# Performance work log

Hardware: AMD Instinct MI355X
Metric: run time of the kernel (lower is better)

Reference implementation:

```python
import jax, jax.numpy as jnp
import numpy as np

HIDDEN = 4096
N_HEADS = 32
N_KV = 8
HEAD_DIM = 128
ROPE_THETA = 10000.0
B, S = 2, 2048


def _rope_neox(x, cos, sin):
    # x: [B,S,H,D]; cos/sin: [B,S,1,D/2]
    half = x.shape[-1] // 2
    x1, x2 = x[..., :half], x[..., half:]
    return jnp.concatenate([x1 * cos - x2 * sin, x2 * cos + x1 * sin], axis=-1)


def setup_inputs() -> dict:
    key = jax.random.key(0)
    k1, k2, k3 = jax.random.split(key, 3)
    hidden_states = jax.random.normal(k1, (B, S, HIDDEN), dtype=jnp.float32)
    positions = jnp.arange(B * S, dtype=jnp.int32).reshape(B, S)
    q_size = N_HEADS * HEAD_DIM
    kv_size = N_KV * HEAD_DIM
    w_qkv = jax.random.normal(k2, (HIDDEN, q_size + 2 * kv_size), dtype=jnp.float32) * (HIDDEN ** -0.5)
    w_o = jax.random.normal(k3, (q_size, HIDDEN), dtype=jnp.float32) * (q_size ** -0.5)
    return {"hidden_states": hidden_states, "positions": positions, "w_qkv": w_qkv, "w_o": w_o}


def reference(hidden_states, positions, w_qkv, w_o):
    q_size = N_HEADS * HEAD_DIM
    kv_size = N_KV * HEAD_DIM
    b, s, _ = hidden_states.shape

    qkv = hidden_states @ w_qkv  # [B,S,q+2kv]
    q = qkv[..., :q_size].reshape(b, s, N_HEADS, HEAD_DIM)
    k = qkv[..., q_size:q_size + kv_size].reshape(b, s, N_KV, HEAD_DIM)
    v = qkv[..., q_size + kv_size:].reshape(b, s, N_KV, HEAD_DIM)

    # RoPE (neox style, full rotary dim)
    inv_freq = 1.0 / (ROPE_THETA ** (jnp.arange(0, HEAD_DIM, 2, dtype=jnp.float32) / HEAD_DIM))
    ang = positions.astype(jnp.float32)[..., None] * inv_freq  # [B,S,D/2]
    cos = jnp.cos(ang)[:, :, None, :]
    sin = jnp.sin(ang)[:, :, None, :]
    q = _rope_neox(q, cos, sin)
    k = _rope_neox(k, cos, sin)

    # GQA: expand kv heads to match q heads
    rep = N_HEADS // N_KV
    k = jnp.repeat(k, rep, axis=2)  # [B,S,H,D]
    v = jnp.repeat(v, rep, axis=2)

    scale = HEAD_DIM ** -0.5
    scores = jnp.einsum('bqhd,bkhd->bhqk', q, k) * scale  # [B,H,S,S]
    causal = jnp.tril(jnp.ones((s, s), dtype=bool))
    scores = jnp.where(causal[None, None], scores, jnp.finfo(scores.dtype).min)
    probs = jax.nn.softmax(scores, axis=-1)
    attn = jnp.einsum('bhqk,bkhd->bqhd', probs, v).reshape(b, s, q_size)
    return attn @ w_o
```

## Files before the change

### kernel.cpp

```cpp
#include <hip/hip_runtime.h>
#include <hip/hip_bf16.h>
#include <stdint.h>
#include <stddef.h>

typedef unsigned short u16;
typedef __bf16 bf16x8 __attribute__((ext_vector_type(8)));
typedef float f32x4 __attribute__((ext_vector_type(4)));
typedef float f32x16 __attribute__((ext_vector_type(16)));
typedef unsigned u32x2 __attribute__((ext_vector_type(2)));

#define NH 32
#define NKV 8
#define HD 128
#define QKV_N 6144
#define SEQ 2048

__device__ __forceinline__ u16 f2b(float x) {
  union { float f; unsigned u; } v; v.f = x;
  unsigned r = v.u + 0x7FFF + ((v.u >> 16) & 1);
  return (u16)(r >> 16);
}
__device__ __forceinline__ float b2f(u16 b) {
  union { float f; unsigned u; } v; v.u = ((unsigned)b) << 16;
  return v.f;
}
__device__ __forceinline__ void gload16(const void* g, void* l) {
  __builtin_amdgcn_global_load_lds((const __attribute__((address_space(1))) unsigned int*)g,
                                   (__attribute__((address_space(3))) unsigned int*)l, 16, 0, 0);
}
template <int N>
__device__ __forceinline__ void vmwait() {
  asm volatile("s_waitcnt vmcnt(%0)" ::"n"(N) : "memory");
}
__device__ __forceinline__ unsigned pk(float lo, float hi) {
  union { __bf16 h[2]; unsigned w; } u;
  u.h[0] = (__bf16)lo; u.h[1] = (__bf16)hi;
  return u.w;
}
__device__ __forceinline__ void plswap(unsigned& a, unsigned& b) {
  u32x2 r = __builtin_amdgcn_permlane32_swap(a, b, false, false);
  a = r.x; b = r.y;
}
__device__ __forceinline__ float pl_partner_max(float x) {
  unsigned u = __float_as_uint(x);
  u32x2 r = __builtin_amdgcn_permlane32_swap(u, u, false, false);
  return fmaxf(__uint_as_float(r.x), __uint_as_float(r.y));
}
__device__ __forceinline__ float pl_partner_sum(float x) {
  unsigned u = __float_as_uint(x);
  u32x2 r = __builtin_amdgcn_permlane32_swap(u, u, false, false);
  return __uint_as_float(r.x) + __uint_as_float(r.y);
}

__global__ void cast_f32_bf16(const float* __restrict__ in, u16* __restrict__ out, int n) {
  int i = (blockIdx.x * blockDim.x + threadIdx.x) * 4;
  if (i >= n) return;
  float4 v = *(const float4*)&in[i];
  ushort4 o;
  o.x = f2b(v.x); o.y = f2b(v.y); o.z = f2b(v.z); o.w = f2b(v.w);
  *(ushort4*)&out[i] = o;
}

__global__ void cast_transpose(const float* __restrict__ in, u16* __restrict__ out, int K, int N) {
  __shared__ float t[32][33];
  int n0 = blockIdx.x * 32, k0 = blockIdx.y * 32;
  int tx = threadIdx.x, ty = threadIdx.y;
#pragma unroll
  for (int i = 0; i < 4; ++i)
    t[ty + i * 8][tx] = in[(size_t)(k0 + ty + i * 8) * N + n0 + tx];
  __syncthreads();
#pragma unroll
  for (int i = 0; i < 4; ++i)
    out[(size_t)(n0 + ty + i * 8) * K + k0 + tx] = f2b(t[tx][ty + i * 8]);
}

__device__ __forceinline__ void storeC(float* C, size_t i, float v) { C[i] = v; }
__device__ __forceinline__ void storeC(u16* C, size_t i, float v) { C[i] = f2b(v); }

#define MFMA16(q, A0, A1, B0, B1)                                                              \
  {                                                                                            \
    _Pragma("unroll") for (int mi = 0; mi < 4; ++mi)                                           \
      _Pragma("unroll") for (int ni = 0; ni < 2; ++ni)                                         \
        acc[q][mi][ni] = __builtin_amdgcn_mfma_f32_16x16x32_bf16(A0[mi], B0[ni], acc[q][mi][ni], 0, 0, 0); \
    _Pragma("unroll") for (int mi = 0; mi < 4; ++mi)                                           \
      _Pragma("unroll") for (int ni = 0; ni < 2; ++ni)                                         \
        acc[q][mi][ni] = __builtin_amdgcn_mfma_f32_16x16x32_bf16(A1[mi], B1[ni], acc[q][mi][ni], 0, 0, 0); \
  }

#define KTILE(NOFF, SGHI, SGLO, VMA, HASVMB, VMB)                                              \
  {                                                                                            \
    bf16x8 a0[4], a1[4], bl0[2], bl1[2], bh0[2], bh1[2];                                       \
                                  \
    _Pragma("unroll") for (int mi = 0; mi < 4; ++mi) {                                         \
      a0[mi] = *(const bf16x8*)(rA0 + (NOFF) + mi * 1024);                                     \
      a1[mi] = *(const bf16x8*)(rA1 + (NOFF) + mi * 1024);                                     \
    }                                                                                          \
    _Pragma("unroll") for (int ni = 0; ni < 2; ++ni) {                                         \
      bl0[ni] = *(const bf16x8*)(rB0 + (NOFF) + ni * 1024);                                    \
      bl1[ni] = *(const bf16x8*)(rB1 + (NOFF) + ni * 1024);                                    \
      bh0[ni] = *(const bf16x8*)(rB0 + (NOFF) + 8192 + ni * 1024);                             \
      bh1[ni] = *(const bf16x8*)(rB1 + (NOFF) + 8192 + ni * 1024);                             \
    }                                                                                          \
    if (SGHI) {                                                                                \
      gload16(pBhi0, dBhi0 + ((NOFF) ^ 16384)); gload16(pBhi1, dBhi1 + ((NOFF) ^ 16384));      \
      pBhi0 += 64; pBhi1 += 64;                                                                \
      gload16(pAhi0, dAhi0 + ((NOFF) ^ 16384)); gload16(pAhi1, dAhi1 + ((NOFF) ^ 16384));      \
      pAhi0 += 64; pAhi1 += 64;                                                                \
    }                                                                                          \
    __builtin_amdgcn_s_barrier();                                                              \
    __builtin_amdgcn_s_setprio(1);                                                             \
    MFMA16(0, a0, a1, bl0, bl1)                                                                \
    MFMA16(1, a0, a1, bh0, bh1)                                                                \
    __builtin_amdgcn_s_setprio(0);                                                             \
    __builtin_amdgcn_sched_barrier(0);                                                         \
    vmwait<VMA>();                                                                             \
    __builtin_amdgcn_s_barrier();                                                              \
                                         \
    _Pragma("unroll") for (int mi = 0; mi < 4; ++mi) {                                         \
      a0[mi] = *(const bf16x8*)(rA0 + (NOFF) + 8192 + mi * 1024);                              \
      a1[mi] = *(const bf16x8*)(rA1 + (NOFF) + 8192 + mi * 1024);                              \
    }                                                                                          \
    if (SGLO) {                                                                                \
      gload16(pAlo0, dAlo0 + (NOFF)); gload16(pAlo1, dAlo1 + (NOFF));                          \
      pAlo0 += 64; pAlo1 += 64;                                                                \
      gload16(pBlo0, dBlo0 + (NOFF)); gload16(pBlo1, dBlo1 + (NOFF));                          \
      pBlo0 += 64; pBlo1 += 64;                                                                \
    }                                                                                          \
    __builtin_amdgcn_s_barrier();                                                              \
    __builtin_amdgcn_s_setprio(1);                                                             \
    MFMA16(2, a0, a1, bl0, bl1)                                                                \
    MFMA16(3, a0, a1, bh0, bh1)                                                                \
    __builtin_amdgcn_s_setprio(0);                                                             \
    __builtin_amdgcn_sched_barrier(0);                                                         \
    if (HASVMB) vmwait<VMB>();                                                                 \
    __builtin_amdgcn_s_barrier();                                                              \
  }

template <typename OutT>
__global__ __launch_bounds__(512, 2) void gemm256(const u16* __restrict__ A, const u16* __restrict__ Bt,
                                                  OutT* __restrict__ C, int M, int N, int K) {
  __shared__ __align__(16) u16 sA[2 * 16384];
  __shared__ __align__(16) u16 sB[2 * 16384];
  const int nbx = N >> 8;
  const int nwg = (M >> 8) * nbx;
  const int cpx = nwg >> 3;
  const int wg = ((int)blockIdx.x & 7) * cpx + ((int)blockIdx.x >> 3);
  const int row0 = (wg / nbx) << 8, col0 = (wg % nbx) << 8;
  const int tid = threadIdx.x, w = tid >> 6, lane = tid & 63;
  const int wm = w >> 2, wn = w & 3;
  const int lq = lane & 15, lh = lane >> 4, x7 = lq & 7;
  const int o0 = (lh ^ x7) << 3, o1 = ((4 + lh) ^ x7) << 3;
  const int nt = K >> 6;

  const int rr = tid >> 3;
  const int swz = ((tid & 7) ^ (rr & 7)) << 3;
  const u16* pAlo0 = A + (size_t)(row0 + rr) * K + swz;
  const u16* pAlo1 = A + (size_t)(row0 + 64 + rr) * K + swz;
  const u16* pAhi0 = A + (size_t)(row0 + 128 + rr) * K + swz;
  const u16* pAhi1 = A + (size_t)(row0 + 192 + rr) * K + swz;
  const u16* pBlo0 = Bt + (size_t)(col0 + rr) * K + swz;
  const u16* pBlo1 = Bt + (size_t)(col0 + 64 + rr) * K + swz;
  const u16* pBhi0 = Bt + (size_t)(col0 + 128 + rr) * K + swz;
  const u16* pBhi1 = Bt + (size_t)(col0 + 192 + rr) * K + swz;
  u16* dAlo0 = sA + w * 512;
  u16* dAlo1 = sA + 4096 + w * 512;
  u16* dAhi0 = sA + 8192 + w * 512;
  u16* dAhi1 = sA + 12288 + w * 512;
  u16* dBlo0 = sB + w * 512;
  u16* dBlo1 = sB + 4096 + w * 512;
  u16* dBhi0 = sB + 8192 + w * 512;
  u16* dBhi1 = sB + 12288 + w * 512;
  const u16* rA0 = sA + (wm * 64 + lq) * 64 + o0;
  const u16* rA1 = sA + (wm * 64 + lq) * 64 + o1;
  const u16* rB0 = sB + (wn * 32 + lq) * 64 + o0;
  const u16* rB1 = sB + (wn * 32 + lq) * 64 + o1;

  f32x4 acc[4][4][2] = {};

  gload16(pAlo0, dAlo0); gload16(pAlo1, dAlo1); pAlo0 += 64; pAlo1 += 64;
  gload16(pBlo0, dBlo0); gload16(pBlo1, dBlo1); pBlo0 += 64; pBlo1 += 64;
  gload16(pBhi0, dBhi0); gload16(pBhi1, dBhi1); pBhi0 += 64; pBhi1 += 64;
  gload16(pAhi0, dAhi0); gload16(pAhi1, dAhi1); pAhi0 += 64; pAhi1 += 64;
  gload16(pAlo0, dAlo0 + 16384); gload16(pAlo1, dAlo1 + 16384); pAlo0 += 64; pAlo1 += 64;
  gload16(pBlo0, dBlo0 + 16384); gload16(pBlo1, dBlo1 + 16384); pBlo0 += 64; pBlo1 += 64;
  vmwait<6>();
  __builtin_amdgcn_s_barrier();

  for (int t = 0; t < nt - 2; t += 2) {
    KTILE(0, 1, 1, 8, 1, 6)
    KTILE(16384, 1, 1, 8, 1, 6)
  }
  KTILE(0, 1, 0, 8, 1, 2)
  KTILE(16384, 0, 0, 0, 0, 0)

#pragma unroll
  for (int q = 0; q < 4; ++q) {
    const int ah = q >> 1, bh2 = q & 1;
#pragma unroll
    for (int mi = 0; mi < 4; ++mi)
#pragma unroll
      for (int ni = 0; ni < 2; ++ni)
#pragma unroll
        for (int j = 0; j < 4; ++j) {
          const int row = row0 + ah * 128 + wm * 64 + mi * 16 + lh * 4 + j;
          const int col = col0 + bh2 * 128 + wn * 32 + ni * 16 + lq;
          storeC(C, (size_t)row * N + col, acc[q][mi][ni][j]);
        }
  }
}

__global__ void rope_kernel(u16* __restrict__ qkv, const int* __restrict__ pos, float qscale) {
  __shared__ float cs[64], sn[64];
  const int row = blockIdx.x;
  const int tid = threadIdx.x;
  if (tid < 64) {
    float p = (float)pos[row];
    float inv = exp2f(-(float)tid * 0.20762050593046f);
    float a = p * inv;
    cs[tid] = cosf(a);
    sn[tid] = sinf(a);
  }
  __syncthreads();
  const size_t base = (size_t)row * QKV_N;
  for (int i = tid; i < 40 * 64; i += 256) {
    const int h = i >> 6, d = i & 63;
    const size_t o = base + h * 128 + d;
    float x1 = b2f(qkv[o]), x2 = b2f(qkv[o + 64]);
    float c = cs[d], s = sn[d];
    float o1 = x1 * c - x2 * s;
    float o2 = x2 * c + x1 * s;
    if (h < NH) { o1 *= qscale; o2 *= qscale; }
    qkv[o] = f2b(o1);
    qkv[o + 64] = f2b(o2);
  }
}

__global__ void v_transpose(const u16* __restrict__ qkv, u16* __restrict__ vt) {
  __shared__ u16 t[32][33];
  const int b = blockIdx.z >> 3, kvh = blockIdx.z & 7;
  const int s0 = blockIdx.x * 32, d0 = blockIdx.y * 32;
  const int tx = threadIdx.x, ty = threadIdx.y;
#pragma unroll
  for (int i = 0; i < 4; ++i)
    t[ty + i * 8][tx] = qkv[(size_t)(b * SEQ + s0 + ty + i * 8) * QKV_N + 5120 + kvh * 128 + d0 + tx];
  __syncthreads();
#pragma unroll
  for (int i = 0; i < 4; ++i)
    vt[(size_t)((b * NKV + kvh) * HD + d0 + ty + i * 8) * SEQ + s0 + tx] = t[tx][ty + i * 8];
}

__global__ __launch_bounds__(512, 2) void attn_kernel(const u16* __restrict__ qkv, const u16* __restrict__ vt,
                                                      u16* __restrict__ attn) {
  __shared__ __align__(16) u16 sK[2][64 * 128];
  __shared__ __align__(16) u16 sV[2][128 * 64];
  const int b = blockIdx.z, h = blockIdx.y;
  const int qt = (b == 0) ? blockIdx.x : 7 - blockIdx.x;
  const int kvh = h >> 2;
  const int qb = qt * 256;
  const int tid = threadIdx.x, w = tid >> 6, lane = tid & 63;
  const int lq = lane & 31, hi = lane >> 5, x7 = lane & 7;
  const int qw = qb + (w << 5);
  const int qa = qw + lq;
  const int nt = 4 * (qt + 1);

  auto stage = [&](int buf, int kt) {
    const int k0 = kt * 64;
#pragma unroll
    for (int c = 0; c < 2; ++c) {
      const int g = c * 512 + tid;
      const int r = g >> 4, gc = g & 15;
      const int gs = gc ^ (r & 7);
      gload16(qkv + (size_t)(b * SEQ + k0 + r) * QKV_N + 4096 + kvh * 128 + gs * 8,
              &sK[buf][(c * 512 + (w << 6)) * 8]);
    }
#pragma unroll
    for (int c = 0; c < 2; ++c) {
      const int g = c * 512 + tid;
      const int r = g >> 3, gc = g & 7;
      const int gs = gc ^ (r & 7);
      gload16(vt + (size_t)((b * NKV + kvh) * HD + r) * SEQ + k0 + gs * 8,
              &sV[buf][(c * 512 + (w << 6)) * 8]);
    }
  };

  stage(0, 0);
  bf16x8 qf[8];
#pragma unroll
  for (int ks = 0; ks < 8; ++ks)
    qf[ks] = *(const bf16x8*)&qkv[(size_t)(b * SEQ + qw + lq) * QKV_N + h * 128 + ks * 16 + 8 * hi];

  f32x16 o[4] = {};
  float mreg = -1e30f, lreg = 0.f;

  asm volatile("s_waitcnt vmcnt(0)" ::: "memory");
  __builtin_amdgcn_s_barrier();

  for (int kt = 0; kt < nt; ++kt) {
    const int cur = kt & 1;
    const int k0 = kt * 64;
    if (kt + 1 < nt) {
      stage(cur ^ 1, kt + 1);
      asm volatile("s_waitcnt vmcnt(4)" ::: "memory");
    } else {
      asm volatile("s_waitcnt vmcnt(0)" ::: "memory");
    }
    __builtin_amdgcn_s_barrier();

    if (k0 <= qw + 31) {
      const u16* sk = sK[cur];
      f32x16 st0 = {}, st1 = {};
      __builtin_amdgcn_s_setprio(1);
#pragma unroll
      for (int ks = 0; ks < 8; ++ks) {
        const int g = ((2 * ks + hi) ^ x7) * 8;
        bf16x8 kf0 = *(const bf16x8*)&sk[lq * 128 + g];
        bf16x8 kf1 = *(const bf16x8*)&sk[(32 + lq) * 128 + g];
        st0 = __builtin_amdgcn_mfma_f32_32x32x16_bf16(kf0, qf[ks], st0, 0, 0, 0);
        st1 = __builtin_amdgcn_mfma_f32_32x32x16_bf16(kf1, qf[ks], st1, 0, 0, 0);
      }
      __builtin_amdgcn_s_setprio(0);
      if (k0 + 63 > qw) {
#pragma unroll
        for (int r = 0; r < 16; ++r) {
          const int cr = (r & 3) + 8 * (r >> 2) + 4 * hi;
          st0[r] = (k0 + cr <= qa) ? st0[r] : -1e30f;
          st1[r] = (k0 + 32 + cr <= qa) ? st1[r] : -1e30f;
        }
      }
      float a8[8];
#pragma unroll
      for (int r = 0; r < 8; ++r)
        a8[r] = fmaxf(fmaxf(st0[r], st0[r + 8]), fmaxf(st1[r], st1[r + 8]));
#pragma unroll
      for (int s = 4; s; s >>= 1)
#pragma unroll
        for (int r = 0; r < s; ++r) a8[r] = fmaxf(a8[r], a8[r + s]);
      const float pm = pl_partner_max(a8[0]);
      if (!__all(pm <= mreg + 8.f)) {
        const float mn = fmaxf(mreg, pm);
        const float al = exp2f(mreg - mn);
        lreg *= al;
        mreg = mn;
#pragma unroll
        for (int r = 0; r < 16; ++r) {
          const int cr = (r & 3) + 8 * (r >> 2) + 4 * hi;
          const float ar = __shfl(al, cr, 64);
#pragma unroll
          for (int dn = 0; dn < 4; ++dn) o[dn][r] *= ar;
        }
      }
#pragma unroll
      for (int r = 0; r < 16; ++r) {
        st0[r] = exp2f(st0[r] - mreg);
        st1[r] = exp2f(st1[r] - mreg);
      }
      float s8[8];
#pragma unroll
      for (int r = 0; r < 8; ++r)
        s8[r] = (st0[r] + st0[r + 8]) + (st1[r] + st1[r + 8]);
#pragma unroll
      for (int s = 4; s; s >>= 1)
#pragma unroll
        for (int r = 0; r < s; ++r) s8[r] += s8[r + s];
      lreg += pl_partner_sum(s8[0]);
      union U8 { unsigned w[4]; bf16x8 v; };
      U8 pa[4];
#define PACKFRAG(F, P0, P1, P2, P3, P4, P5, P6, P7)                   \
      {                                                               \
        unsigned a0 = pk(P0, P1), a1 = pk(P2, P3);                    \
        unsigned b0 = pk(P4, P5), b1 = pk(P6, P7);                    \
        plswap(a0, b0); plswap(a1, b1);                               \
        pa[F].w[0] = a0; pa[F].w[1] = a1; pa[F].w[2] = b0; pa[F].w[3] = b1; \
      }
      PACKFRAG(0, st0[0], st0[1], st0[2], st0[3], st0[4], st0[5], st0[6], st0[7])
      PACKFRAG(1, st0[8], st0[9], st0[10], st0[11], st0[12], st0[13], st0[14], st0[15])
      PACKFRAG(2, st1[0], st1[1], st1[2], st1[3], st1[4], st1[5], st1[6], st1[7])
      PACKFRAG(3, st1[8], st1[9], st1[10], st1[11], st1[12], st1[13], st1[14], st1[15])
#undef PACKFRAG
      const u16* sv = sV[cur];
      __builtin_amdgcn_s_setprio(1);
#pragma unroll
      for (int dn = 0; dn < 4; ++dn) {
#pragma unroll
        for (int ks = 0; ks < 4; ++ks) {
          bf16x8 vf = *(const bf16x8*)&sv[(dn * 32 + lq) * 64 + (((2 * ks + hi) ^ x7)) * 8];
          o[dn] = __builtin_amdgcn_mfma_f32_32x32x16_bf16(pa[ks].v, vf, o[dn], 0, 0, 0);
        }
      }
      __builtin_amdgcn_s_setprio(0);
    }
    __builtin_amdgcn_s_barrier();
  }

  const float inv = 1.0f / lreg;
#pragma unroll
  for (int r = 0; r < 16; ++r) {
    const int cr = (r & 3) + 8 * (r >> 2) + 4 * hi;
    const float fr = __shfl(inv, cr, 64);
    const size_t row = (size_t)(b * SEQ + qw + cr);
#pragma unroll
    for (int dn = 0; dn < 4; ++dn)
      attn[row * 4096 + h * 128 + dn * 32 + lq] = f2b(o[dn][r] * fr);
  }
}

extern "C" void kernel_launch(void* const* d_in, const int* in_sizes, int n_in,
                              void* d_out, int out_size, void* d_ws, size_t ws_size,
                              hipStream_t stream) {
  const float* hs = (const float*)d_in[0];
  const int* pos = (const int*)d_in[1];
  const float* w_qkv = (const float*)d_in[2];
  const float* w_o = (const float*)d_in[3];
  float* out = (float*)d_out;
  char* ws = (char*)d_ws;

  u16* hid = (u16*)ws;
  u16* attnb = hid;
  u16* wT = (u16*)(ws + 33554432);
  u16* qkv = (u16*)(ws + 83886080);
  u16* vt = (u16*)(ws + 134217728);

  const float qscale = 0.12751744f;

  cast_f32_bf16<<<16384, 256, 0, stream>>>(hs, hid, 4096 * 4096);
  cast_transpose<<<dim3(192, 128), dim3(32, 8), 0, stream>>>(w_qkv, wT, 4096, QKV_N);
  gemm256<u16><<<384, 512, 0, stream>>>(hid, wT, qkv, 4096, QKV_N, 4096);
  rope_kernel<<<4096, 256, 0, stream>>>(qkv, pos, qscale);
  v_transpose<<<dim3(64, 4, 16), dim3(32, 8), 0, stream>>>(qkv, vt);
  cast_transpose<<<dim3(128, 128), dim3(32, 8), 0, stream>>>(w_o, wT, 4096, 4096);
  attn_kernel<<<dim3(8, 32, 2), 512, 0, stream>>>(qkv, vt, attnb);
  gemm256<float><<<256, 512, 0, stream>>>(attnb, wT, out, 4096, 4096, 4096);
}
```

Baseline: 545.3 us.

## Add 256x192-tile GEMM for QKV projection to balance work across CUs

Adds a new gemm192 kernel that uses 256x192 output tiles with its own double-buffered LDS pipeline and launch bounds allowing two workgroups per CU, and uses it for the QKV projection instead of the 256x256 gemm256. The QKV GEMM becomes 512 workgroups instead of 384, which should fill the 256 CUs more evenly and cut wave-quantization tail time. In exchange, each tile reuses operands less and has a different load/wait schedule, which could lower per-tile MFMA efficiency or cause LDS/register pressure.

```diff
diff --git a/kernel.cpp b/kernel.cpp
--- a/kernel.cpp
+++ b/kernel.cpp
@@ -90,7 +90,6 @@
 #define KTILE(NOFF, SGHI, SGLO, VMA, HASVMB, VMB)                                              \
   {                                                                                            \
     bf16x8 a0[4], a1[4], bl0[2], bl1[2], bh0[2], bh1[2];                                       \
-                                  \
     _Pragma("unroll") for (int mi = 0; mi < 4; ++mi) {                                         \
       a0[mi] = *(const bf16x8*)(rA0 + (NOFF) + mi * 1024);                                     \
       a1[mi] = *(const bf16x8*)(rA1 + (NOFF) + mi * 1024);                                     \
@@ -115,7 +114,6 @@
     __builtin_amdgcn_sched_barrier(0);                                                         \
     vmwait<VMA>();                                                                             \
     __builtin_amdgcn_s_barrier();                                                              \
-                                         \
     _Pragma("unroll") for (int mi = 0; mi < 4; ++mi) {                                         \
       a0[mi] = *(const bf16x8*)(rA0 + (NOFF) + 8192 + mi * 1024);                              \
       a1[mi] = *(const bf16x8*)(rA1 + (NOFF) + 8192 + mi * 1024);                              \
@@ -209,6 +207,126 @@
   }
 }
 
+#define MM24(q, A0, A1)                                                                        \
+  {                                                                                            \
+    _Pragma("unroll") for (int mi = 0; mi < 4; ++mi)                                           \
+      _Pragma("unroll") for (int ni = 0; ni < 3; ++ni)                                         \
+        acc[q][mi][ni] = __builtin_amdgcn_mfma_f32_16x16x32_bf16(A0[mi], b0[ni], acc[q][mi][ni], 0, 0, 0); \
+    _Pragma("unroll") for (int mi = 0; mi < 4; ++mi)                                           \
+      _Pragma("unroll") for (int ni = 0; ni < 3; ++ni)                                         \
+        acc[q][mi][ni] = __builtin_amdgcn_mfma_f32_16x16x32_bf16(A1[mi], b1[ni], acc[q][mi][ni], 0, 0, 0); \
+  }
+
+#define KT192(NA, NB, SGHI, SGLO, HASV0, HASV1, VM1)                                           \
+  {                                                                                            \
+    bf16x8 a0[4], a1[4], b0[3], b1[3];                                                         \
+                                \
+    _Pragma("unroll") for (int mi = 0; mi < 4; ++mi) {                                         \
+      a0[mi] = *(const bf16x8*)(rA0 + (NA) + mi * 1024);                                       \
+      a1[mi] = *(const bf16x8*)(rA1 + (NA) + mi * 1024);                                       \
+    }                                                                                          \
+    _Pragma("unroll") for (int ni = 0; ni < 3; ++ni) {                                         \
+      b0[ni] = *(const bf16x8*)(rB0 + (NB) + ni * 1024);                                       \
+      b1[ni] = *(const bf16x8*)(rB1 + (NB) + ni * 1024);                                       \
+    }                                                                                          \
+    if (SGHI) {                                                                                \
+      gload16(pA2, dA2 + ((NA) ^ 16384)); gload16(pA3, dA3 + ((NA) ^ 16384));                  \
+      pA2 += 64; pA3 += 64;                                                                    \
+      gload16(pB0, dB0 + ((NB) ^ 12288)); gload16(pB1, dB1 + ((NB) ^ 12288));                  \
+      gload16(pB2, dB2 + ((NB) ^ 12288));                                                      \
+      pB0 += 64; pB1 += 64; pB2 += 64;                                                         \
+    }                                                                                          \
+    __builtin_amdgcn_s_barrier();                                                              \
+    __builtin_amdgcn_s_setprio(1);                                                             \
+    MM24(0, a0, a1)                                                                            \
+    __builtin_amdgcn_s_setprio(0);                                                             \
+    __builtin_amdgcn_sched_barrier(0);                                                         \
+    if (HASV0) vmwait<7>();                                                                    \
+    __builtin_amdgcn_s_barrier();                                                              \
+                                                    \
+    _Pragma("unroll") for (int mi = 0; mi < 4; ++mi) {                                         \
+      a0[mi] = *(const bf16x8*)(rA0 + (NA) + 8192 + mi * 1024);                                \
+      a1[mi] = *(const bf16x8*)(rA1 + (NA) + 8192 + mi * 1024);                                \
+    }                                                                                          \
+    if (SGLO) {                                                                                \
+      gload16(pA0, dA0 + (NA)); gload16(pA1, dA1 + (NA));                                      \
+      pA0 += 64; pA1 += 64;                                                                    \
+    }                                                                                          \
+    __builtin_amdgcn_s_barrier();                                                              \
+    __builtin_amdgcn_s_setprio(1);                                                             \
+    MM24(1, a0, a1)                                                                            \
+    __builtin_amdgcn_s_setprio(0);                                                             \
+    __builtin_amdgcn_sched_barrier(0);                                                         \
+    if (HASV1) vmwait<VM1>();                                                                  \
+    __builtin_amdgcn_s_barrier();                                                              \
+  }
+
+__global__ __launch_bounds__(512, 2) void gemm192(const u16* __restrict__ A, const u16* __restrict__ Bt,
+                                                  u16* __restrict__ C, int M, int N, int K) {
+  __shared__ __align__(16) u16 sA[2 * 16384];
+  __shared__ __align__(16) u16 sB[2 * 12288];
+  const int nbx = N / 192;
+  const int nwg = (M >> 8) * nbx;
+  const int cpx = nwg >> 3;
+  const int wg = ((int)blockIdx.x & 7) * cpx + ((int)blockIdx.x >> 3);
+  const int row0 = (wg / nbx) << 8, col0 = (wg % nbx) * 192;
+  const int tid = threadIdx.x, w = tid >> 6, lane = tid & 63;
+  const int wm = w >> 2, wn = w & 3;
+  const int lq = lane & 15, lh = lane >> 4, x7 = lq & 7;
+  const int o0 = (lh ^ x7) << 3, o1 = ((4 + lh) ^ x7) << 3;
+  const int nt = K >> 6;
+
+  const int rr = tid >> 3;
+  const int swz = ((tid & 7) ^ (rr & 7)) << 3;
+  const u16* pA0 = A + (size_t)(row0 + rr) * K + swz;
+  const u16* pA1 = A + (size_t)(row0 + 64 + rr) * K + swz;
+  const u16* pA2 = A + (size_t)(row0 + 128 + rr) * K + swz;
+  const u16* pA3 = A + (size_t)(row0 + 192 + rr) * K + swz;
+  const u16* pB0 = Bt + (size_t)(col0 + rr) * K + swz;
+  const u16* pB1 = Bt + (size_t)(col0 + 64 + rr) * K + swz;
+  const u16* pB2 = Bt + (size_t)(col0 + 128 + rr) * K + swz;
+  u16* dA0 = sA + w * 512;
+  u16* dA1 = sA + 4096 + w * 512;
+  u16* dA2 = sA + 8192 + w * 512;
+  u16* dA3 = sA + 12288 + w * 512;
+  u16* dB0 = sB + w * 512;
+  u16* dB1 = sB + 4096 + w * 512;
+  u16* dB2 = sB + 8192 + w * 512;
+  const u16* rA0 = sA + (wm * 64 + lq) * 64 + o0;
+  const u16* rA1 = sA + (wm * 64 + lq) * 64 + o1;
+  const u16* rB0 = sB + (wn * 48 + lq) * 64 + o0;
+  const u16* rB1 = sB + (wn * 48 + lq) * 64 + o1;
+
+  f32x4 acc[2][4][3] = {};
+
+  gload16(pA0, dA0); gload16(pA1, dA1); pA0 += 64; pA1 += 64;
+  gload16(pB0, dB0); gload16(pB1, dB1); gload16(pB2, dB2); pB0 += 64; pB1 += 64; pB2 += 64;
+  gload16(pA2, dA2); gload16(pA3, dA3); pA2 += 64; pA3 += 64;
+  gload16(pA0, dA0 + 16384); gload16(pA1, dA1 + 16384); pA0 += 64; pA1 += 64;
+  vmwait<4>();
+  __builtin_amdgcn_s_barrier();
+
+  for (int t = 0; t < nt - 2; t += 2) {
+    KT192(0, 0, 1, 1, 1, 1, 2)
+    KT192(16384, 12288, 1, 1, 1, 1, 2)
+  }
+  KT192(0, 0, 1, 0, 1, 1, 0)
+  KT192(16384, 12288, 0, 0, 0, 0, 0)
+
+#pragma unroll
+  for (int ah = 0; ah < 2; ++ah)
+#pragma unroll
+    for (int mi = 0; mi < 4; ++mi)
+#pragma unroll
+      for (int ni = 0; ni < 3; ++ni)
+#pragma unroll
+        for (int j = 0; j < 4; ++j) {
+          const int row = row0 + ah * 128 + wm * 64 + mi * 16 + lh * 4 + j;
+          const int col = col0 + wn * 48 + ni * 16 + lq;
+          C[(size_t)row * N + col] = f2b(acc[ah][mi][ni][j]);
+        }
+}
+
 __global__ void rope_kernel(u16* __restrict__ qkv, const int* __restrict__ pos, float qscale) {
   __shared__ float cs[64], sn[64];
   const int row = blockIdx.x;
@@ -424,7 +542,7 @@
 
   cast_f32_bf16<<<16384, 256, 0, stream>>>(hs, hid, 4096 * 4096);
   cast_transpose<<<dim3(192, 128), dim3(32, 8), 0, stream>>>(w_qkv, wT, 4096, QKV_N);
-  gemm256<u16><<<384, 512, 0, stream>>>(hid, wT, qkv, 4096, QKV_N, 4096);
+  gemm192<<<512, 512, 0, stream>>>(hid, wT, qkv, 4096, QKV_N, 4096);
   rope_kernel<<<4096, 256, 0, stream>>>(qkv, pos, qscale);
   v_transpose<<<dim3(64, 4, 16), dim3(32, 8), 0, stream>>>(qkv, vt);
   cast_transpose<<<dim3(128, 128), dim3(32, 8), 0, stream>>>(w_o, wT, 4096, 4096);
```

Result: faster. 520.9 us (-4.5%).
